# Kernel tuning notes

Measured on AMD Instinct MI355X. Metric: run time of the kernel, lower is better.

The kernel has to match this reference:

```python
import jax, jax.numpy as jnp
import numpy as np

EPS = 1e-12
SAMPLE_SIZES = (100, 50)  # hardcoded in the torch module


def setup_inputs() -> dict:
    key = jax.random.key(0)
    k1, k2, k3, k4 = jax.random.split(key, 4)
    N, E, C_IN, C_HID, C_OUT = 50000, 1600000, 256, 64, 128
    x = jax.random.normal(k1, (N, C_IN), dtype=jnp.float32)
    edge_index = jax.random.randint(k2, (2, E), 0, N, dtype=jnp.int64)
    W1 = jax.random.normal(k3, (C_IN, C_HID), dtype=jnp.float32) / np.sqrt(C_IN)
    b1 = jnp.zeros((C_HID,), dtype=jnp.float32)
    W2 = jax.random.normal(k4, (C_HID, C_OUT), dtype=jnp.float32) / np.sqrt(C_HID)
    b2 = jnp.zeros((C_OUT,), dtype=jnp.float32)
    return {"x": x, "edge_index": edge_index, "W1": W1, "b1": b1, "W2": W2, "b2": b2}


def _sample_mask(edge_index, num_samples, key):
    """Keep at most num_samples random out-edges per source node (fixed-shape mask)."""
    src = edge_index[0]
    E = src.shape[0]
    pri = jax.random.uniform(key, (E,))
    order = jnp.lexsort((pri, src))            # group by src, random order within group
    src_sorted = src[order]
    first = jnp.searchsorted(src_sorted, src_sorted, side="left")
    rank = jnp.arange(E) - first               # rank within each src group
    keep_sorted = rank < num_samples
    mask = jnp.zeros((E,), dtype=jnp.float32).at[order].set(keep_sorted.astype(jnp.float32))
    return mask


def _gcn_conv(x, edge_index, edge_weight, W, b, num_nodes):
    """PyG GCNConv: self-loops + symmetric deg^-1/2 normalization, aggregate at dst."""
    h = x @ W                                   # [N, out]
    src, dst = edge_index[0], edge_index[1]
    loop = jnp.arange(num_nodes, dtype=src.dtype)
    src_f = jnp.concatenate([src, loop])
    dst_f = jnp.concatenate([dst, loop])
    w_f = jnp.concatenate([edge_weight, jnp.ones((num_nodes,), dtype=edge_weight.dtype)])
    deg = jax.ops.segment_sum(w_f, dst_f, num_segments=num_nodes)
    dinv = jnp.where(deg > 0, jax.lax.rsqrt(jnp.maximum(deg, EPS)), 0.0)
    norm = w_f * dinv[src_f] * dinv[dst_f]      # [E+N]
    msgs = h[src_f] * norm[:, None]             # gather + scale (memory bound)
    out = jax.ops.segment_sum(msgs, dst_f, num_segments=num_nodes)
    return out + b


def reference(x, edge_index, W1, b1, W2, b2):
    num_nodes = x.shape[0]
    skey = jax.random.key(42)
    sk1, sk2 = jax.random.split(skey)
    m1 = _sample_mask(edge_index, SAMPLE_SIZES[0], sk1)
    m2 = _sample_mask(edge_index, SAMPLE_SIZES[1], sk2)
    h = _gcn_conv(x, edge_index, m1, W1, b1, num_nodes)
    h = jax.nn.relu(h)
    h = h / jnp.maximum(jnp.linalg.norm(h, axis=-1, keepdims=True), EPS)  # F.normalize(p=2)
    out = _gcn_conv(h, edge_index, m2, W2, b2, num_nodes)
    return out
```

## Files before the change

kernel.cpp:

```cpp
#include <hip/hip_runtime.h>

typedef unsigned int u32;
typedef unsigned short u16;
typedef unsigned long long u64;
typedef __attribute__((ext_vector_type(8))) short bh8;
typedef __attribute__((ext_vector_type(4))) float f4;

#define HMAX 1024
#define MAXD 128
#define SB_CAP 24576
#define SBCHUNK 2048
#define SPLIT 8

__device__ inline f4 mfma16(bh8 a, bh8 b, f4 c) {
  return __builtin_amdgcn_mfma_f32_16x16x32_bf16(a, b, c, 0, 0, 0);
}

__host__ __device__ inline void tf2x32(u32 k0, u32 k1, u32 x0, u32 x1, u32& o0, u32& o1) {
  u32 ks2 = k0 ^ k1 ^ 0x1BD11BDAu;
#define ROTL32(x,d) (((x)<<(d))|((x)>>(32-(d))))
#define TFR(r) { x0 += x1; x1 = ROTL32(x1,(r)); x1 ^= x0; }
  x0 += k0; x1 += k1;
  TFR(13) TFR(15) TFR(26) TFR(6)
  x0 += k1; x1 += ks2 + 1u;
  TFR(17) TFR(29) TFR(16) TFR(24)
  x0 += ks2; x1 += k0 + 2u;
  TFR(13) TFR(15) TFR(26) TFR(6)
  x0 += k0; x1 += k1 + 3u;
  TFR(17) TFR(29) TFR(16) TFR(24)
  x0 += k1; x1 += ks2 + 4u;
  TFR(13) TFR(15) TFR(26) TFR(6)
  x0 += ks2; x1 += k0 + 5u;
  o0 = x0; o1 = x1;
#undef TFR
#undef ROTL32
}

__device__ inline u16 f2bf(float f) {
  u32 u = __float_as_uint(f);
  return (u16)((u + 0x7FFFu + ((u >> 16) & 1u)) >> 16);
}
__device__ inline float bflo(u32 u) { return __uint_as_float(u << 16); }
__device__ inline float bfhi(u32 u) { return __uint_as_float(u & 0xFFFF0000u); }

__global__ __launch_bounds__(256) void k_prep(const float* __restrict__ W1, const float* __restrict__ W2,
                                              u16* __restrict__ W1t, u16* __restrict__ W2t) {
  int t = blockIdx.x * 256 + threadIdx.x;
  for (int e = t; e < 256 * 64; e += 1024) {
    int n = e & 63, k = e >> 6;
    W1t[n * 256 + k] = f2bf(W1[k * 64 + n]);
  }
  for (int e = t; e < 64 * 128; e += 1024) {
    int n = e & 127, k = e >> 7;
    W2t[n * 64 + k] = f2bf(W2[k * 128 + n]);
  }
}

__global__ __launch_bounds__(256) void k_srcbin(const int* __restrict__ ei,
                                                int* __restrict__ srcCnt, u32* __restrict__ srcRec,
                                                int* __restrict__ dstCnt, int E, int nb) {
  __shared__ u32 lsrc[128], ldst[128], lbase[128];
  int t = threadIdx.x;
  if (t < 128) { lsrc[t] = 0; ldst[t] = 0; }
  __syncthreads();
  int lo = blockIdx.x * SBCHUNK;
  int hi = min(lo + SBCHUNK, E);
  int sv[SBCHUNK / 256];
  int ci = 0;
  for (int i = lo + t; i < hi; i += 256) {
    int s = ei[i];
    int d = ei[E + i];
    sv[ci++] = s;
    atomicAdd(&lsrc[s >> 9], 1u);
    atomicAdd(&ldst[d >> 9], 1u);
  }
  __syncthreads();
  if (t < 128) {
    u32 c = lsrc[t];
    if (c) lbase[t] = (u32)atomicAdd(&srcCnt[t], (int)c);
    lsrc[t] = 0;
    if (ldst[t]) atomicAdd(&dstCnt[t], (int)ldst[t]);
  }
  __syncthreads();
  ci = 0;
  for (int i = lo + t; i < hi; i += 256) {
    int s = sv[ci++];
    int bk = s >> 9;
    u32 slot = lbase[bk] + atomicAdd(&lsrc[bk], 1u);
    if (slot < SB_CAP)
      srcRec[(size_t)bk * SB_CAP + slot] = ((u32)(s & 511) << 21) | (u32)i;
  }
}

__global__ __launch_bounds__(256) void k_shist(const int* __restrict__ srcCnt, const u32* __restrict__ srcRec,
                                               int* __restrict__ outdegB) {
  int bk = blockIdx.x >> 3;
  int part = blockIdx.x & (SPLIT - 1);
  int total = min(srcCnt[bk], SB_CAP);
  int lo = total * part / SPLIT;
  int hi = total * (part + 1) / SPLIT;
  __shared__ u32 cnt[512];
  int t = threadIdx.x;
  cnt[t] = 0; cnt[t + 256] = 0;
  __syncthreads();
  const u32* R = srcRec + (size_t)bk * SB_CAP;
  for (int i = lo + t; i < hi; i += 256) atomicAdd(&cnt[R[i] >> 21], 1u);
  __syncthreads();
  int base = bk * 512;
  for (int v = t; v < 512; v += 256) {
    u32 c = cnt[v];
    if (c) atomicAdd(&outdegB[base + v], (int)c);
  }
}

__global__ __launch_bounds__(256) void k_hdetect(const int* __restrict__ outdegB, u32* __restrict__ idAB,
                                                 int* __restrict__ hcA, int* __restrict__ hcB,
                                                 const int* __restrict__ dstCnt, int* __restrict__ bucketBase,
                                                 int* __restrict__ bucketCur, int* __restrict__ dptr,
                                                 int nb, int N) {
  if (blockIdx.x == 0 && threadIdx.x == 0) {
    int s = 0;
    for (int i = 0; i < nb; ++i) { bucketBase[i] = s; bucketCur[i] = s; s += dstCnt[i]; }
    bucketBase[nb] = s;
    dptr[N] = s;
  }
  int v = blockIdx.x * 256 + threadIdx.x;
  if (v >= N) return;
  int dg = outdegB[v];
  u32 pk = 0;
  if (dg > 50) {
    int idb = atomicAdd(hcB, 1);
    if (idb < HMAX) pk = (u32)(idb + 1);
    if (dg > 100) {
      int ida = atomicAdd(hcA, 1);
      if (ida < HMAX) pk |= (u32)(ida + 1) << 16;
    }
  }
  idAB[v] = pk;
}

__global__ __launch_bounds__(256) void k_hfill(const int* __restrict__ srcCnt, const u32* __restrict__ srcRec,
                                               const u32* __restrict__ idAB,
                                               int* __restrict__ bcA, u64* __restrict__ bukA,
                                               int* __restrict__ bcB, u64* __restrict__ bukB,
                                               u32 kaA, u32 kbA, u32 kaB, u32 kbB) {
  int bk = blockIdx.x >> 3;
  int part = blockIdx.x & (SPLIT - 1);
  int total = min(srcCnt[bk], SB_CAP);
  int lo = total * part / SPLIT;
  int hi = total * (part + 1) / SPLIT;
  const u32* R = srcRec + (size_t)bk * SB_CAP;
  int base = bk * 512;
  for (int i = lo + threadIdx.x; i < hi; i += 256) {
    u32 r = R[i];
    u32 pk = idAB[base + (int)(r >> 21)];
    if (pk) {
      u32 e = r & 0x1FFFFFu;
      int idb = (int)(pk & 0xFFFFu) - 1;
      if (idb >= 0) {
        u32 w0, w1; tf2x32(kaB, kbB, 0u, e, w0, w1);
        int slot = atomicAdd(&bcB[idb], 1);
        if (slot < MAXD) bukB[(size_t)idb * MAXD + slot] = ((u64)((w0 ^ w1) >> 9) << 32) | e;
      }
      int ida = (int)(pk >> 16) - 1;
      if (ida >= 0) {
        u32 w0, w1; tf2x32(kaA, kbA, 0u, e, w0, w1);
        int slot = atomicAdd(&bcA[ida], 1);
        if (slot < MAXD) bukA[(size_t)ida * MAXD + slot] = ((u64)((w0 ^ w1) >> 9) << 32) | e;
      }
    }
  }
}

__global__ __launch_bounds__(256) void k_rank2(const int* __restrict__ hcA, const int* __restrict__ bcA,
                                               const u64* __restrict__ bukA,
                                               const int* __restrict__ hcB, const int* __restrict__ bcB,
                                               const u64* __restrict__ bukB,
                                               unsigned char* __restrict__ mask) {
  bool isA = blockIdx.x < (HMAX / 4);
  int bx = isA ? blockIdx.x : blockIdx.x - HMAX / 4;
  const int* hcount = isA ? hcA : hcB;
  const int* bcount = isA ? bcA : bcB;
  const u64* bucket = isA ? bukA : bukB;
  int S = isA ? 100 : 50;
  int bit = isA ? 1 : 2;
  int wid = (bx * 256 + (int)threadIdx.x) >> 6;
  int lane = threadIdx.x & 63;
  int hc = hcount[0]; if (hc > HMAX) hc = HMAX;
  if (wid >= hc) return;
  int d = bcount[wid]; if (d > MAXD) d = MAXD;
  const u64* B = bucket + (size_t)wid * MAXD;
  for (int i = lane; i < d; i += 64) {
    u64 ki = B[i];
    int rank = 0;
    for (int j = 0; j < d; ++j) rank += (B[j] < ki) ? 1 : 0;
    if (rank >= S) {
      u32 e = (u32)ki;
      mask[e] = (unsigned char)(mask[e] & ~bit);
    }
  }
}

#define P1CHUNK 8192
__global__ __launch_bounds__(256) void k_phase1(const int* __restrict__ ei,
                                                const unsigned char* __restrict__ mask,
                                                int* __restrict__ bucketCur, u32* __restrict__ records, int E) {
  __shared__ u32 lc[128];
  __shared__ u32 lbase[128];
  int t = threadIdx.x;
  if (t < 128) lc[t] = 0;
  __syncthreads();
  int lo = blockIdx.x * P1CHUNK;
  int hi = min(lo + P1CHUNK, E);
  for (int i = lo + t; i < hi; i += 256) {
    int d = ei[E + i];
    atomicAdd(&lc[d >> 9], 1u);
  }
  __syncthreads();
  if (t < 128) {
    u32 c = lc[t];
    if (c) lbase[t] = (u32)atomicAdd(&bucketCur[t], (int)c);
    lc[t] = 0;
  }
  __syncthreads();
  for (int i = lo + t; i < hi; i += 256) {
    int s = ei[i];
    int d = ei[E + i];
    unsigned char m = mask[i];
    int bk = d >> 9;
    u32 slot = lbase[bk] + atomicAdd(&lc[bk], 1u);
    records[slot] = (u32)s | ((u32)(d & 511) << 16) | ((u32)(m & 3u) << 25);
  }
}

__global__ __launch_bounds__(256) void k_phase2(const int* __restrict__ bucketBase,
                                                const u32* __restrict__ records,
                                                u32* __restrict__ entries, int* __restrict__ dptr,
                                                float* __restrict__ dinv1, float* __restrict__ dinv2, int N) {
  int b = blockIdx.x;
  int lo = bucketBase[b], hi = bucketBase[b + 1];
  __shared__ u32 cnt[512];
  __shared__ u32 ws4[4];
  int t = threadIdx.x;
  cnt[t] = 0; cnt[t + 256] = 0;
  __syncthreads();
  for (int i = lo + t; i < hi; i += 256) {
    u32 r = records[i];
    u32 dl = (r >> 16) & 511u;
    u32 add = 1u + (((r >> 25) & 1u) << 10) + (((r >> 26) & 1u) << 20);
    atomicAdd(&cnt[dl], add);
  }
  __syncthreads();
  u32 c0 = cnt[2 * t], c1 = cnt[2 * t + 1];
  u32 n0 = c0 & 1023u, n1 = c1 & 1023u;
  u32 pair = n0 + n1;
  int lane = t & 63, w = t >> 6;
  u32 incl = pair;
  for (int off = 1; off < 64; off <<= 1) {
    u32 nbv = (u32)__shfl_up((int)incl, off, 64);
    if (lane >= off) incl += nbv;
  }
  if (lane == 63) ws4[w] = incl;
  __syncthreads();
  if (t == 0) { u32 s = 0; for (int k = 0; k < 4; ++k) { u32 x = ws4[k]; ws4[k] = s; s += x; } }
  __syncthreads();
  u32 excl = incl - pair + ws4[w];
  int v0 = b * 512 + 2 * t;
  if (v0 < N) {
    dptr[v0] = lo + (int)excl;
    dinv1[v0] = 1.0f / sqrtf((float)(((c0 >> 10) & 1023u) + 1u));
    dinv2[v0] = 1.0f / sqrtf((float)(((c0 >> 20) & 1023u) + 1u));
  }
  if (v0 + 1 < N) {
    dptr[v0 + 1] = lo + (int)(excl + n0);
    dinv1[v0 + 1] = 1.0f / sqrtf((float)(((c1 >> 10) & 1023u) + 1u));
    dinv2[v0 + 1] = 1.0f / sqrtf((float)(((c1 >> 20) & 1023u) + 1u));
  }
  __syncthreads();
  cnt[2 * t] = excl;
  cnt[2 * t + 1] = excl + n0;
  __syncthreads();
  for (int i = lo + t; i < hi; i += 256) {
    u32 r = records[i];
    u32 dl = (r >> 16) & 511u;
    u32 slot = atomicAdd(&cnt[dl], 1u);
    entries[lo + slot] = (r & 0xFFFFu) | ((r & (1u << 25)) ? (1u << 30) : 0u)
                                       | ((r & (1u << 26)) ? (1u << 31) : 0u);
  }
}

#define G1S 136
__global__ __launch_bounds__(256) void k_gemm1(const float* __restrict__ x, const u16* __restrict__ W1t,
                                               u16* __restrict__ h1b, int N) {
  __shared__ u16 xs[64 * G1S];
  __shared__ u16 ws[64 * G1S];
  int t = threadIdx.x;
  int wv = t >> 6, lane = t & 63;
  int qd = lane >> 4, md = lane & 15;
  int m0 = blockIdx.x * 64;
  f4 acc[4] = {};
  for (int ks = 0; ks < 256; ks += 128) {
    __syncthreads();
#pragma unroll
    for (int i = 0; i < 8; ++i) {
      int f = t + 256 * i;
      int r = f >> 5, c4 = f & 31;
      int grow = m0 + r; if (grow >= N) grow = N - 1;
      float4 v = ((const float4*)x)[(size_t)grow * 64 + (ks >> 2) + c4];
      u32 p0 = (u32)f2bf(v.x) | ((u32)f2bf(v.y) << 16);
      u32 p1 = (u32)f2bf(v.z) | ((u32)f2bf(v.w) << 16);
      *((uint2*)(xs + r * G1S + c4 * 4)) = make_uint2(p0, p1);
    }
#pragma unroll
    for (int i = 0; i < 4; ++i) {
      int cc = t + 256 * i;
      int n = cc >> 4, kc = (cc & 15) * 8;
      *((uint4*)(ws + n * G1S + kc)) = *((const uint4*)(W1t + n * 256 + ks + kc));
    }
    __syncthreads();
#pragma unroll
    for (int kk = 0; kk < 128; kk += 32) {
      bh8 af = *((const bh8*)(xs + (16 * wv + md) * G1S + kk + qd * 8));
#pragma unroll
      for (int nt = 0; nt < 4; ++nt) {
        bh8 bf = *((const bh8*)(ws + (nt * 16 + md) * G1S + kk + qd * 8));
        acc[nt] = mfma16(af, bf, acc[nt]);
      }
    }
  }
#pragma unroll
  for (int nt = 0; nt < 4; ++nt)
#pragma unroll
    for (int r = 0; r < 4; ++r) {
      int row = m0 + 16 * wv + qd * 4 + r;
      if (row < N) h1b[(size_t)row * 64 + nt * 16 + md] = f2bf(acc[nt][r]);
    }
}

__global__ __launch_bounds__(256) void k_conv1n(const int* __restrict__ ptr, const u32* __restrict__ entries,
                                                const float* __restrict__ dinv1, const uint4* __restrict__ h1q,
                                                const float* __restrict__ b1, uint4* __restrict__ hnbq, int N) {
  int wid = (blockIdx.x * 256 + threadIdx.x) >> 6;
  if (wid >= N) return;
  int lane = threadIdx.x & 63;
  int lo8 = lane & 7, grp = lane >> 3;
  int beg = ptr[wid], end = ptr[wid + 1];
  float a0 = 0.f, a1 = 0.f, a2 = 0.f, a3 = 0.f, a4 = 0.f, a5 = 0.f, a6 = 0.f, a7 = 0.f;
  for (int cb = beg; cb < end; cb += 64) {
    int idx = cb + lane;
    float wgt = 0.f; int s = 0;
    if (idx < end) {
      u32 e = entries[idx];
      s = (int)(e & 0xFFFFu);
      if (e & (1u << 30)) wgt = dinv1[s];
    }
    int nq = (min(64, end - cb) + 7) >> 3;
    int j = grp;
    float w = __shfl(wgt, j, 64);
    int sj = __shfl(s, j, 64);
    uint4 uv = h1q[(size_t)sj * 8 + lo8];
    for (int i = 1; i < nq; ++i) {
      int j2 = j + 8;
      float w2 = __shfl(wgt, j2, 64);
      int s2 = __shfl(s, j2, 64);
      uint4 uv2 = h1q[(size_t)s2 * 8 + lo8];
      a0 = fmaf(w, bflo(uv.x), a0); a1 = fmaf(w, bfhi(uv.x), a1);
      a2 = fmaf(w, bflo(uv.y), a2); a3 = fmaf(w, bfhi(uv.y), a3);
      a4 = fmaf(w, bflo(uv.z), a4); a5 = fmaf(w, bfhi(uv.z), a5);
      a6 = fmaf(w, bflo(uv.w), a6); a7 = fmaf(w, bfhi(uv.w), a7);
      w = w2; uv = uv2; j = j2;
    }
    a0 = fmaf(w, bflo(uv.x), a0); a1 = fmaf(w, bfhi(uv.x), a1);
    a2 = fmaf(w, bflo(uv.y), a2); a3 = fmaf(w, bfhi(uv.y), a3);
    a4 = fmaf(w, bflo(uv.z), a4); a5 = fmaf(w, bfhi(uv.z), a5);
    a6 = fmaf(w, bflo(uv.w), a6); a7 = fmaf(w, bfhi(uv.w), a7);
  }
#pragma unroll
  for (int off = 8; off < 64; off <<= 1) {
    a0 += __shfl_xor(a0, off, 64); a1 += __shfl_xor(a1, off, 64);
    a2 += __shfl_xor(a2, off, 64); a3 += __shfl_xor(a3, off, 64);
    a4 += __shfl_xor(a4, off, 64); a5 += __shfl_xor(a5, off, 64);
    a6 += __shfl_xor(a6, off, 64); a7 += __shfl_xor(a7, off, 64);
  }
  float dv = dinv1[wid];
  uint4 uo = h1q[(size_t)wid * 8 + lo8];
  a0 = fmaf(dv, bflo(uo.x), a0); a1 = fmaf(dv, bfhi(uo.x), a1);
  a2 = fmaf(dv, bflo(uo.y), a2); a3 = fmaf(dv, bfhi(uo.y), a3);
  a4 = fmaf(dv, bflo(uo.z), a4); a5 = fmaf(dv, bfhi(uo.z), a5);
  a6 = fmaf(dv, bflo(uo.w), a6); a7 = fmaf(dv, bfhi(uo.w), a7);
  float4 bbA = ((const float4*)b1)[lo8 * 2];
  float4 bbB = ((const float4*)b1)[lo8 * 2 + 1];
  float o0 = fmaxf(fmaf(dv, a0, bbA.x), 0.f);
  float o1 = fmaxf(fmaf(dv, a1, bbA.y), 0.f);
  float o2 = fmaxf(fmaf(dv, a2, bbA.z), 0.f);
  float o3 = fmaxf(fmaf(dv, a3, bbA.w), 0.f);
  float o4 = fmaxf(fmaf(dv, a4, bbB.x), 0.f);
  float o5 = fmaxf(fmaf(dv, a5, bbB.y), 0.f);
  float o6 = fmaxf(fmaf(dv, a6, bbB.z), 0.f);
  float o7 = fmaxf(fmaf(dv, a7, bbB.w), 0.f);
  float ss = fmaf(o0, o0, fmaf(o1, o1, fmaf(o2, o2, o3 * o3)))
           + fmaf(o4, o4, fmaf(o5, o5, fmaf(o6, o6, o7 * o7)));
#pragma unroll
  for (int off = 1; off < 8; off <<= 1) ss += __shfl_xor(ss, off, 8);
  float sc = 1.f / fmaxf(sqrtf(ss), 1e-12f);
  if (lane < 8) {
    uint4 pv;
    pv.x = (u32)f2bf(o0 * sc) | ((u32)f2bf(o1 * sc) << 16);
    pv.y = (u32)f2bf(o2 * sc) | ((u32)f2bf(o3 * sc) << 16);
    pv.z = (u32)f2bf(o4 * sc) | ((u32)f2bf(o5 * sc) << 16);
    pv.w = (u32)f2bf(o6 * sc) | ((u32)f2bf(o7 * sc) << 16);
    hnbq[(size_t)wid * 8 + lo8] = pv;
  }
}

__global__ __launch_bounds__(256) void k_agg2(const int* __restrict__ ptr, const u32* __restrict__ entries,
                                              const float* __restrict__ dinv2, const uint4* __restrict__ hnq,
                                              uint4* __restrict__ agg2q, int N) {
  int wid = (blockIdx.x * 256 + threadIdx.x) >> 6;
  if (wid >= N) return;
  int lane = threadIdx.x & 63;
  int lo8 = lane & 7, grp = lane >> 3;
  int beg = ptr[wid], end = ptr[wid + 1];
  float a0 = 0.f, a1 = 0.f, a2 = 0.f, a3 = 0.f, a4 = 0.f, a5 = 0.f, a6 = 0.f, a7 = 0.f;
  for (int cb = beg; cb < end; cb += 64) {
    int idx = cb + lane;
    float wgt = 0.f; int s = 0;
    if (idx < end) {
      u32 e = entries[idx];
      s = (int)(e & 0xFFFFu);
      if (e & (1u << 31)) wgt = dinv2[s];
    }
    int nq = (min(64, end - cb) + 7) >> 3;
    int j = grp;
    float w = __shfl(wgt, j, 64);
    int sj = __shfl(s, j, 64);
    uint4 uv = hnq[(size_t)sj * 8 + lo8];
    for (int i = 1; i < nq; ++i) {
      int j2 = j + 8;
      float w2 = __shfl(wgt, j2, 64);
      int s2 = __shfl(s, j2, 64);
      uint4 uv2 = hnq[(size_t)s2 * 8 + lo8];
      a0 = fmaf(w, bflo(uv.x), a0); a1 = fmaf(w, bfhi(uv.x), a1);
      a2 = fmaf(w, bflo(uv.y), a2); a3 = fmaf(w, bfhi(uv.y), a3);
      a4 = fmaf(w, bflo(uv.z), a4); a5 = fmaf(w, bfhi(uv.z), a5);
      a6 = fmaf(w, bflo(uv.w), a6); a7 = fmaf(w, bfhi(uv.w), a7);
      w = w2; uv = uv2; j = j2;
    }
    a0 = fmaf(w, bflo(uv.x), a0); a1 = fmaf(w, bfhi(uv.x), a1);
    a2 = fmaf(w, bflo(uv.y), a2); a3 = fmaf(w, bfhi(uv.y), a3);
    a4 = fmaf(w, bflo(uv.z), a4); a5 = fmaf(w, bfhi(uv.z), a5);
    a6 = fmaf(w, bflo(uv.w), a6); a7 = fmaf(w, bfhi(uv.w), a7);
  }
#pragma unroll
  for (int off = 8; off < 64; off <<= 1) {
    a0 += __shfl_xor(a0, off, 64); a1 += __shfl_xor(a1, off, 64);
    a2 += __shfl_xor(a2, off, 64); a3 += __shfl_xor(a3, off, 64);
    a4 += __shfl_xor(a4, off, 64); a5 += __shfl_xor(a5, off, 64);
    a6 += __shfl_xor(a6, off, 64); a7 += __shfl_xor(a7, off, 64);
  }
  float dv = dinv2[wid];
  uint4 uo = hnq[(size_t)wid * 8 + lo8];
  a0 = fmaf(dv, bflo(uo.x), a0); a1 = fmaf(dv, bfhi(uo.x), a1);
  a2 = fmaf(dv, bflo(uo.y), a2); a3 = fmaf(dv, bfhi(uo.y), a3);
  a4 = fmaf(dv, bflo(uo.z), a4); a5 = fmaf(dv, bfhi(uo.z), a5);
  a6 = fmaf(dv, bflo(uo.w), a6); a7 = fmaf(dv, bfhi(uo.w), a7);
  if (lane < 8) {
    uint4 pv;
    pv.x = (u32)f2bf(dv * a0) | ((u32)f2bf(dv * a1) << 16);
    pv.y = (u32)f2bf(dv * a2) | ((u32)f2bf(dv * a3) << 16);
    pv.z = (u32)f2bf(dv * a4) | ((u32)f2bf(dv * a5) << 16);
    pv.w = (u32)f2bf(dv * a6) | ((u32)f2bf(dv * a7) << 16);
    agg2q[(size_t)wid * 8 + lo8] = pv;
  }
}

#define G2S 72
__global__ __launch_bounds__(256) void k_gemm2f(const u16* __restrict__ aggb, const u16* __restrict__ W2t,
                                                const float* __restrict__ b2, float* __restrict__ out, int N) {
  __shared__ u16 hs[64 * G2S];
  __shared__ u16 ws[128 * G2S];
  int t = threadIdx.x;
  int wv = t >> 6, lane = t & 63;
  int qd = lane >> 4, md = lane & 15;
  int m0 = blockIdx.x * 64;
#pragma unroll
  for (int i = 0; i < 2; ++i) {
    int cc = t + 256 * i;
    int r = cc >> 3, kc = (cc & 7) * 8;
    int grow = m0 + r; if (grow >= N) grow = N - 1;
    *((uint4*)(hs + r * G2S + kc)) = *((const uint4*)(aggb + (size_t)grow * 64 + kc));
  }
#pragma unroll
  for (int i = 0; i < 4; ++i) {
    int cc = t + 256 * i;
    int n = cc >> 3, kc = (cc & 7) * 8;
    *((uint4*)(ws + n * G2S + kc)) = *((const uint4*)(W2t + n * 64 + kc));
  }
  __syncthreads();
  f4 acc[8] = {};
#pragma unroll
  for (int kk = 0; kk < 64; kk += 32) {
    bh8 af = *((const bh8*)(hs + (16 * wv + md) * G2S + kk + qd * 8));
#pragma unroll
    for (int nt = 0; nt < 8; ++nt) {
      bh8 bf = *((const bh8*)(ws + (nt * 16 + md) * G2S + kk + qd * 8));
      acc[nt] = mfma16(af, bf, acc[nt]);
    }
  }
#pragma unroll
  for (int nt = 0; nt < 8; ++nt) {
    float bv = b2[nt * 16 + md];
#pragma unroll
    for (int r = 0; r < 4; ++r) {
      int row = m0 + 16 * wv + qd * 4 + r;
      if (row < N) out[(size_t)row * 128 + nt * 16 + md] = acc[nt][r] + bv;
    }
  }
}

extern "C" void kernel_launch(void* const* d_in, const int* in_sizes, int n_in,
                              void* d_out, int out_size, void* d_ws, size_t ws_size,
                              hipStream_t stream) {
  const float* x  = (const float*)d_in[0];
  const int*   ei = (const int*)d_in[1];
  const float* W1 = (const float*)d_in[2];
  const float* b1 = (const float*)d_in[3];
  const float* W2 = (const float*)d_in[4];
  const float* b2 = (const float*)d_in[5];
  const int N = in_sizes[0] / 256;
  const int E = in_sizes[1] / 2;
  const int nb = (N + 511) >> 9;

  u32 sk1a, sk1b, sk2a, sk2b;
  tf2x32(0u, 42u, 0u, 0u, sk1a, sk1b);
  tf2x32(0u, 42u, 0u, 1u, sk2a, sk2b);

  char* p = (char*)d_ws;
  auto alloc = [&](size_t bytes) { char* r = p; p += (bytes + 255) & ~(size_t)255; return r; };
  int* dstCnt      = (int*)alloc(128 * 4);
  int* srcCnt      = (int*)alloc(128 * 4);
  int* hcbA        = (int*)alloc((size_t)(1 + HMAX) * 4);
  int* hcbB        = (int*)alloc((size_t)(1 + HMAX) * 4);
  int* outdegB     = (int*)alloc((size_t)nb * 512 * 4);
  char* zero_end = p;
  unsigned char* mask = (unsigned char*)alloc((size_t)E);
  u32* idAB     = (u32*)alloc((size_t)nb * 512 * 4);
  u16* h1b      = (u16*)alloc((size_t)N * 64 * 2);
  u16* hnb      = (u16*)alloc((size_t)N * 64 * 2);
  u16* agg2b    = (u16*)alloc((size_t)N * 64 * 2);
  float* dinv1  = (float*)alloc((size_t)N * 4);
  float* dinv2  = (float*)alloc((size_t)N * 4);
  int* dptr     = (int*)alloc((size_t)(N + 1) * 4);
  int* bucketBase = (int*)alloc(129 * 4);
  int* bucketCur  = (int*)alloc(128 * 4);
  u32* records  = (u32*)alloc((size_t)E * 4);
  u32* entries  = (u32*)alloc((size_t)E * 4);
  u32* srcRec   = (u32*)alloc((size_t)nb * SB_CAP * 4);
  u64* bukA     = (u64*)alloc((size_t)HMAX * MAXD * 8);
  u64* bukB     = (u64*)alloc((size_t)HMAX * MAXD * 8);
  u16* W1t      = (u16*)alloc(256 * 64 * 2);
  u16* W2t      = (u16*)alloc(64 * 128 * 2);

  int* hcA = hcbA; int* bcA = hcbA + 1;
  int* hcB = hcbB; int* bcB = hcbB + 1;

  hipMemsetAsync(dstCnt, 0x00, (size_t)(zero_end - (char*)dstCnt), stream);
  hipMemsetAsync(mask, 0x03, (size_t)E, stream);

  k_prep<<<4, 256, 0, stream>>>(W1, W2, W1t, W2t);
  k_srcbin<<<(E + SBCHUNK - 1) / SBCHUNK, 256, 0, stream>>>(ei, srcCnt, srcRec, dstCnt, E, nb);
  k_shist<<<nb * SPLIT, 256, 0, stream>>>(srcCnt, srcRec, outdegB);
  k_hdetect<<<(N + 255) / 256, 256, 0, stream>>>(outdegB, idAB, hcA, hcB, dstCnt, bucketBase,
                                                 bucketCur, dptr, nb, N);
  k_hfill<<<nb * SPLIT, 256, 0, stream>>>(srcCnt, srcRec, idAB, bcA, bukA, bcB, bukB,
                                          sk1a, sk1b, sk2a, sk2b);
  k_rank2<<<HMAX / 2, 256, 0, stream>>>(hcA, bcA, bukA, hcB, bcB, bukB, mask);
  k_phase1<<<(E + P1CHUNK - 1) / P1CHUNK, 256, 0, stream>>>(ei, mask, bucketCur, records, E);
  k_phase2<<<nb, 256, 0, stream>>>(bucketBase, records, entries, dptr, dinv1, dinv2, N);

  k_gemm1<<<(N + 63) / 64, 256, 0, stream>>>(x, W1t, h1b, N);
  k_conv1n<<<(N * 64 + 255) / 256, 256, 0, stream>>>(dptr, entries, dinv1, (const uint4*)h1b, b1,
                                                     (uint4*)hnb, N);
  k_agg2<<<(N * 64 + 255) / 256, 256, 0, stream>>>(dptr, entries, dinv2, (const uint4*)hnb,
                                                   (uint4*)agg2b, N);
  k_gemm2f<<<(N + 63) / 64, 256, 0, stream>>>(agg2b, W2t, b2, (float*)d_out, N);
}
```

Baseline: 313.3 us.

## Fuse edge binning, GEMM1 and weight prep into one heterogeneous kernel; drop phase1

Merges the src-binning kernel, the first GEMM and the W2 transpose into one launch, with blocks dispatched by index to different roles so the independent GEMM runs concurrently with the edge binning. The binning now also scatters destination-keyed records (dst, src, edge id) into capped per-bucket slots, which removes the separate phase1 pass that re-read the edge list. Phase2 reads the mask per edge via the stored edge id. W1 is transposed into shared memory inside the GEMM blocks, eliminating the prep kernel. The trade-offs are wider 64-bit records, a random mask gather, and truncation at SB_CAP per destination bucket.

```diff
diff --git a/kernel.cpp b/kernel.cpp
--- a/kernel.cpp
+++ b/kernel.cpp
@@ -11,6 +11,7 @@
 #define SB_CAP 24576
 #define SBCHUNK 2048
 #define SPLIT 8
+#define G1S 136
 
 __device__ inline f4 mfma16(bh8 a, bh8 b, f4 c) {
   return __builtin_amdgcn_mfma_f32_16x16x32_bf16(a, b, c, 0, 0, 0);
@@ -43,52 +44,116 @@
 __device__ inline float bflo(u32 u) { return __uint_as_float(u << 16); }
 __device__ inline float bfhi(u32 u) { return __uint_as_float(u & 0xFFFF0000u); }
 
-__global__ __launch_bounds__(256) void k_prep(const float* __restrict__ W1, const float* __restrict__ W2,
-                                              u16* __restrict__ W1t, u16* __restrict__ W2t) {
-  int t = blockIdx.x * 256 + threadIdx.x;
-  for (int e = t; e < 256 * 64; e += 1024) {
-    int n = e & 63, k = e >> 6;
-    W1t[n * 256 + k] = f2bf(W1[k * 64 + n]);
-  }
-  for (int e = t; e < 64 * 128; e += 1024) {
-    int n = e & 127, k = e >> 7;
-    W2t[n * 64 + k] = f2bf(W2[k * 128 + n]);
-  }
-}
-
-__global__ __launch_bounds__(256) void k_srcbin(const int* __restrict__ ei,
-                                                int* __restrict__ srcCnt, u32* __restrict__ srcRec,
-                                                int* __restrict__ dstCnt, int E, int nb) {
-  __shared__ u32 lsrc[128], ldst[128], lbase[128];
+struct BinS { u32 lsrc[128]; u32 lbase[128]; u32 ldst[128]; u32 dbase[128]; };
+struct GemS { u16 xs[64 * G1S]; u16 ws[64 * G1S]; };
+
+__global__ __launch_bounds__(256) void k_mega1(const int* __restrict__ ei, int E,
+                                               const float* __restrict__ x, int N,
+                                               const float* __restrict__ W1, const float* __restrict__ W2,
+                                               int* __restrict__ srcCnt, u32* __restrict__ srcRec,
+                                               int* __restrict__ dstCnt, u64* __restrict__ dstRec,
+                                               u16* __restrict__ h1b, u16* __restrict__ W2t, int nBin) {
+  __shared__ __align__(16) char smem[sizeof(GemS)];
   int t = threadIdx.x;
-  if (t < 128) { lsrc[t] = 0; ldst[t] = 0; }
-  __syncthreads();
-  int lo = blockIdx.x * SBCHUNK;
-  int hi = min(lo + SBCHUNK, E);
-  int sv[SBCHUNK / 256];
-  int ci = 0;
-  for (int i = lo + t; i < hi; i += 256) {
-    int s = ei[i];
-    int d = ei[E + i];
-    sv[ci++] = s;
-    atomicAdd(&lsrc[s >> 9], 1u);
-    atomicAdd(&ldst[d >> 9], 1u);
-  }
-  __syncthreads();
-  if (t < 128) {
-    u32 c = lsrc[t];
-    if (c) lbase[t] = (u32)atomicAdd(&srcCnt[t], (int)c);
-    lsrc[t] = 0;
-    if (ldst[t]) atomicAdd(&dstCnt[t], (int)ldst[t]);
-  }
-  __syncthreads();
-  ci = 0;
-  for (int i = lo + t; i < hi; i += 256) {
-    int s = sv[ci++];
-    int bk = s >> 9;
-    u32 slot = lbase[bk] + atomicAdd(&lsrc[bk], 1u);
-    if (slot < SB_CAP)
-      srcRec[(size_t)bk * SB_CAP + slot] = ((u32)(s & 511) << 21) | (u32)i;
+  int bid = blockIdx.x;
+
+  if (bid < nBin) {
+    BinS& S = *(BinS*)smem;
+    if (t < 128) { S.lsrc[t] = 0; S.ldst[t] = 0; }
+    __syncthreads();
+    int lo = bid * SBCHUNK;
+    int hi = min(lo + SBCHUNK, E);
+    int e0 = lo + 8 * t;
+    int nv = min(8, hi - e0); if (nv < 0) nv = 0;
+    int sv[8], dv[8];
+    if (nv == 8 && ((E & 3) == 0)) {
+      int4 a0 = *((const int4*)(ei + e0));
+      int4 a1 = *((const int4*)(ei + e0 + 4));
+      int4 b0 = *((const int4*)(ei + E + e0));
+      int4 b1 = *((const int4*)(ei + E + e0 + 4));
+      sv[0]=a0.x; sv[1]=a0.y; sv[2]=a0.z; sv[3]=a0.w; sv[4]=a1.x; sv[5]=a1.y; sv[6]=a1.z; sv[7]=a1.w;
+      dv[0]=b0.x; dv[1]=b0.y; dv[2]=b0.z; dv[3]=b0.w; dv[4]=b1.x; dv[5]=b1.y; dv[6]=b1.z; dv[7]=b1.w;
+    } else {
+      for (int j = 0; j < nv; ++j) { sv[j] = ei[e0 + j]; dv[j] = ei[E + e0 + j]; }
+    }
+    for (int j = 0; j < nv; ++j) {
+      atomicAdd(&S.lsrc[sv[j] >> 9], 1u);
+      atomicAdd(&S.ldst[dv[j] >> 9], 1u);
+    }
+    __syncthreads();
+    if (t < 128) {
+      u32 c = S.lsrc[t];
+      if (c) S.lbase[t] = (u32)atomicAdd(&srcCnt[t], (int)c);
+      S.lsrc[t] = 0;
+      u32 cd = S.ldst[t];
+      if (cd) S.dbase[t] = (u32)atomicAdd(&dstCnt[t], (int)cd);
+      S.ldst[t] = 0;
+    }
+    __syncthreads();
+    for (int j = 0; j < nv; ++j) {
+      int s = sv[j], d = dv[j];
+      u32 i = (u32)(e0 + j);
+      int bs = s >> 9;
+      u32 slot = S.lbase[bs] + atomicAdd(&S.lsrc[bs], 1u);
+      if (slot < SB_CAP) srcRec[(size_t)bs * SB_CAP + slot] = ((u32)(s & 511) << 21) | i;
+      int bd = d >> 9;
+      u32 slot2 = S.dbase[bd] + atomicAdd(&S.ldst[bd], 1u);
+      if (slot2 < SB_CAP)
+        dstRec[(size_t)bd * SB_CAP + slot2] = ((u64)(d & 511) << 37) | ((u64)(u32)s << 21) | i;
+    }
+  } else if (bid < 2 * nBin) {
+    GemS& G = *(GemS*)smem;
+    int wv = t >> 6, lane = t & 63;
+    int qd = lane >> 4, md = lane & 15;
+    int m0 = (bid - nBin) * 64;
+    if (m0 >= N) return;
+    f4 acc[4] = {};
+    for (int ks = 0; ks < 256; ks += 128) {
+      __syncthreads();
+#pragma unroll
+      for (int i = 0; i < 8; ++i) {
+        int f = t + 256 * i;
+        int r = f >> 5, c4 = f & 31;
+        int grow = m0 + r; if (grow >= N) grow = N - 1;
+        float4 v = ((const float4*)x)[(size_t)grow * 64 + (ks >> 2) + c4];
+        u32 p0 = (u32)f2bf(v.x) | ((u32)f2bf(v.y) << 16);
+        u32 p1 = (u32)f2bf(v.z) | ((u32)f2bf(v.w) << 16);
+        *((uint2*)(G.xs + r * G1S + c4 * 4)) = make_uint2(p0, p1);
+      }
+#pragma unroll
+      for (int i = 0; i < 8; ++i) {
+        int f = t + 256 * i;
+        int k = f >> 4, c4 = f & 15;
+        float4 v = ((const float4*)W1)[(ks + k) * 16 + c4];
+        int n0 = c4 * 4;
+        G.ws[(n0 + 0) * G1S + k] = f2bf(v.x);
+        G.ws[(n0 + 1) * G1S + k] = f2bf(v.y);
+        G.ws[(n0 + 2) * G1S + k] = f2bf(v.z);
+        G.ws[(n0 + 3) * G1S + k] = f2bf(v.w);
+      }
+      __syncthreads();
+#pragma unroll
+      for (int kk = 0; kk < 128; kk += 32) {
+        bh8 af = *((const bh8*)(G.xs + (16 * wv + md) * G1S + kk + qd * 8));
+#pragma unroll
+        for (int nt = 0; nt < 4; ++nt) {
+          bh8 bf = *((const bh8*)(G.ws + (nt * 16 + md) * G1S + kk + qd * 8));
+          acc[nt] = mfma16(af, bf, acc[nt]);
+        }
+      }
+    }
+#pragma unroll
+    for (int nt = 0; nt < 4; ++nt)
+#pragma unroll
+      for (int r = 0; r < 4; ++r) {
+        int row = m0 + 16 * wv + qd * 4 + r;
+        if (row < N) h1b[(size_t)row * 64 + nt * 16 + md] = f2bf(acc[nt][r]);
+      }
+  } else {
+    for (int e = t; e < 64 * 128; e += 256) {
+      int n = e & 127, k = e >> 7;
+      W2t[n * 64 + k] = f2bf(W2[k * 128 + n]);
+    }
   }
 }
 
@@ -116,11 +181,10 @@
 __global__ __launch_bounds__(256) void k_hdetect(const int* __restrict__ outdegB, u32* __restrict__ idAB,
                                                  int* __restrict__ hcA, int* __restrict__ hcB,
                                                  const int* __restrict__ dstCnt, int* __restrict__ bucketBase,
-                                                 int* __restrict__ bucketCur, int* __restrict__ dptr,
-                                                 int nb, int N) {
+                                                 int* __restrict__ dptr, int nb, int N) {
   if (blockIdx.x == 0 && threadIdx.x == 0) {
     int s = 0;
-    for (int i = 0; i < nb; ++i) { bucketBase[i] = s; bucketCur[i] = s; s += dstCnt[i]; }
+    for (int i = 0; i < nb; ++i) { bucketBase[i] = s; s += min(dstCnt[i], SB_CAP); }
     bucketBase[nb] = s;
     dptr[N] = s;
   }
@@ -201,53 +265,26 @@
   }
 }
 
-#define P1CHUNK 8192
-__global__ __launch_bounds__(256) void k_phase1(const int* __restrict__ ei,
+__global__ __launch_bounds__(256) void k_phase2(const int* __restrict__ bucketBase,
+                                                const int* __restrict__ dstCnt,
+                                                const u64* __restrict__ dstRec,
                                                 const unsigned char* __restrict__ mask,
-                                                int* __restrict__ bucketCur, u32* __restrict__ records, int E) {
-  __shared__ u32 lc[128];
-  __shared__ u32 lbase[128];
-  int t = threadIdx.x;
-  if (t < 128) lc[t] = 0;
-  __syncthreads();
-  int lo = blockIdx.x * P1CHUNK;
-  int hi = min(lo + P1CHUNK, E);
-  for (int i = lo + t; i < hi; i += 256) {
-    int d = ei[E + i];
-    atomicAdd(&lc[d >> 9], 1u);
-  }
-  __syncthreads();
-  if (t < 128) {
-    u32 c = lc[t];
-    if (c) lbase[t] = (u32)atomicAdd(&bucketCur[t], (int)c);
-    lc[t] = 0;
-  }
-  __syncthreads();
-  for (int i = lo + t; i < hi; i += 256) {
-    int s = ei[i];
-    int d = ei[E + i];
-    unsigned char m = mask[i];
-    int bk = d >> 9;
-    u32 slot = lbase[bk] + atomicAdd(&lc[bk], 1u);
-    records[slot] = (u32)s | ((u32)(d & 511) << 16) | ((u32)(m & 3u) << 25);
-  }
-}
-
-__global__ __launch_bounds__(256) void k_phase2(const int* __restrict__ bucketBase,
-                                                const u32* __restrict__ records,
                                                 u32* __restrict__ entries, int* __restrict__ dptr,
                                                 float* __restrict__ dinv1, float* __restrict__ dinv2, int N) {
   int b = blockIdx.x;
-  int lo = bucketBase[b], hi = bucketBase[b + 1];
+  int base = bucketBase[b];
+  int cnt0 = min(dstCnt[b], SB_CAP);
+  const u64* R = dstRec + (size_t)b * SB_CAP;
   __shared__ u32 cnt[512];
   __shared__ u32 ws4[4];
   int t = threadIdx.x;
   cnt[t] = 0; cnt[t + 256] = 0;
   __syncthreads();
-  for (int i = lo + t; i < hi; i += 256) {
-    u32 r = records[i];
-    u32 dl = (r >> 16) & 511u;
-    u32 add = 1u + (((r >> 25) & 1u) << 10) + (((r >> 26) & 1u) << 20);
+  for (int i = t; i < cnt0; i += 256) {
+    u64 r = R[i];
+    u32 dl = (u32)(r >> 37) & 511u;
+    u32 m = mask[(u32)r & 0x1FFFFFu];
+    u32 add = 1u + ((m & 1u) << 10) + (((m >> 1) & 1u) << 20);
     atomicAdd(&cnt[dl], add);
   }
   __syncthreads();
@@ -267,12 +304,12 @@
   u32 excl = incl - pair + ws4[w];
   int v0 = b * 512 + 2 * t;
   if (v0 < N) {
-    dptr[v0] = lo + (int)excl;
+    dptr[v0] = base + (int)excl;
     dinv1[v0] = 1.0f / sqrtf((float)(((c0 >> 10) & 1023u) + 1u));
     dinv2[v0] = 1.0f / sqrtf((float)(((c0 >> 20) & 1023u) + 1u));
   }
   if (v0 + 1 < N) {
-    dptr[v0 + 1] = lo + (int)(excl + n0);
+    dptr[v0 + 1] = base + (int)(excl + n0);
     dinv1[v0 + 1] = 1.0f / sqrtf((float)(((c1 >> 10) & 1023u) + 1u));
     dinv2[v0 + 1] = 1.0f / sqrtf((float)(((c1 >> 20) & 1023u) + 1u));
   }
@@ -280,61 +317,14 @@
   cnt[2 * t] = excl;
   cnt[2 * t + 1] = excl + n0;
   __syncthreads();
-  for (int i = lo + t; i < hi; i += 256) {
-    u32 r = records[i];
-    u32 dl = (r >> 16) & 511u;
+  for (int i = t; i < cnt0; i += 256) {
+    u64 r = R[i];
+    u32 dl = (u32)(r >> 37) & 511u;
+    u32 m = mask[(u32)r & 0x1FFFFFu];
+    u32 src = (u32)(r >> 21) & 0xFFFFu;
     u32 slot = atomicAdd(&cnt[dl], 1u);
-    entries[lo + slot] = (r & 0xFFFFu) | ((r & (1u << 25)) ? (1u << 30) : 0u)
-                                       | ((r & (1u << 26)) ? (1u << 31) : 0u);
-  }
-}
-
-#define G1S 136
-__global__ __launch_bounds__(256) void k_gemm1(const float* __restrict__ x, const u16* __restrict__ W1t,
-                                               u16* __restrict__ h1b, int N) {
-  __shared__ u16 xs[64 * G1S];
-  __shared__ u16 ws[64 * G1S];
-  int t = threadIdx.x;
-  int wv = t >> 6, lane = t & 63;
-  int qd = lane >> 4, md = lane & 15;
-  int m0 = blockIdx.x * 64;
-  f4 acc[4] = {};
-  for (int ks = 0; ks < 256; ks += 128) {
-    __syncthreads();
-#pragma unroll
-    for (int i = 0; i < 8; ++i) {
-      int f = t + 256 * i;
-      int r = f >> 5, c4 = f & 31;
-      int grow = m0 + r; if (grow >= N) grow = N - 1;
-      float4 v = ((const float4*)x)[(size_t)grow * 64 + (ks >> 2) + c4];
-      u32 p0 = (u32)f2bf(v.x) | ((u32)f2bf(v.y) << 16);
-      u32 p1 = (u32)f2bf(v.z) | ((u32)f2bf(v.w) << 16);
-      *((uint2*)(xs + r * G1S + c4 * 4)) = make_uint2(p0, p1);
-    }
-#pragma unroll
-    for (int i = 0; i < 4; ++i) {
-      int cc = t + 256 * i;
-      int n = cc >> 4, kc = (cc & 15) * 8;
-      *((uint4*)(ws + n * G1S + kc)) = *((const uint4*)(W1t + n * 256 + ks + kc));
-    }
-    __syncthreads();
-#pragma unroll
-    for (int kk = 0; kk < 128; kk += 32) {
-      bh8 af = *((const bh8*)(xs + (16 * wv + md) * G1S + kk + qd * 8));
-#pragma unroll
-      for (int nt = 0; nt < 4; ++nt) {
-        bh8 bf = *((const bh8*)(ws + (nt * 16 + md) * G1S + kk + qd * 8));
-        acc[nt] = mfma16(af, bf, acc[nt]);
-      }
-    }
-  }
-#pragma unroll
-  for (int nt = 0; nt < 4; ++nt)
-#pragma unroll
-    for (int r = 0; r < 4; ++r) {
-      int row = m0 + 16 * wv + qd * 4 + r;
-      if (row < N) h1b[(size_t)row * 64 + nt * 16 + md] = f2bf(acc[nt][r]);
-    }
+    entries[base + slot] = src | ((m & 1u) ? (1u << 30) : 0u) | ((m & 2u) ? (1u << 31) : 0u);
+  }
 }
 
 __global__ __launch_bounds__(256) void k_conv1n(const int* __restrict__ ptr, const u32* __restrict__ entries,
@@ -552,13 +542,11 @@
   float* dinv2  = (float*)alloc((size_t)N * 4);
   int* dptr     = (int*)alloc((size_t)(N + 1) * 4);
   int* bucketBase = (int*)alloc(129 * 4);
-  int* bucketCur  = (int*)alloc(128 * 4);
-  u32* records  = (u32*)alloc((size_t)E * 4);
   u32* entries  = (u32*)alloc((size_t)E * 4);
   u32* srcRec   = (u32*)alloc((size_t)nb * SB_CAP * 4);
+  u64* dstRec   = (u64*)alloc((size_t)nb * SB_CAP * 8);
   u64* bukA     = (u64*)alloc((size_t)HMAX * MAXD * 8);
   u64* bukB     = (u64*)alloc((size_t)HMAX * MAXD * 8);
-  u16* W1t      = (u16*)alloc(256 * 64 * 2);
   u16* W2t      = (u16*)alloc(64 * 128 * 2);
 
   int* hcA = hcbA; int* bcA = hcbA + 1;
@@ -567,18 +555,18 @@
   hipMemsetAsync(dstCnt, 0x00, (size_t)(zero_end - (char*)dstCnt), stream);
   hipMemsetAsync(mask, 0x03, (size_t)E, stream);
 
-  k_prep<<<4, 256, 0, stream>>>(W1, W2, W1t, W2t);
-  k_srcbin<<<(E + SBCHUNK - 1) / SBCHUNK, 256, 0, stream>>>(ei, srcCnt, srcRec, dstCnt, E, nb);
+  const int nBin = (E + SBCHUNK - 1) / SBCHUNK;
+  const int nGemm = (N + 63) / 64;
+  k_mega1<<<nBin + nGemm + 1, 256, 0, stream>>>(ei, E, x, N, W1, W2,
+                                                srcCnt, srcRec, dstCnt, dstRec, h1b, W2t, nBin);
   k_shist<<<nb * SPLIT, 256, 0, stream>>>(srcCnt, srcRec, outdegB);
   k_hdetect<<<(N + 255) / 256, 256, 0, stream>>>(outdegB, idAB, hcA, hcB, dstCnt, bucketBase,
-                                                 bucketCur, dptr, nb, N);
+                                                 dptr, nb, N);
   k_hfill<<<nb * SPLIT, 256, 0, stream>>>(srcCnt, srcRec, idAB, bcA, bukA, bcB, bukB,
                                           sk1a, sk1b, sk2a, sk2b);
   k_rank2<<<HMAX / 2, 256, 0, stream>>>(hcA, bcA, bukA, hcB, bcB, bukB, mask);
-  k_phase1<<<(E + P1CHUNK - 1) / P1CHUNK, 256, 0, stream>>>(ei, mask, bucketCur, records, E);
-  k_phase2<<<nb, 256, 0, stream>>>(bucketBase, records, entries, dptr, dinv1, dinv2, N);
-
-  k_gemm1<<<(N + 63) / 64, 256, 0, stream>>>(x, W1t, h1b, N);
+  k_phase2<<<nb, 256, 0, stream>>>(bucketBase, dstCnt, dstRec, mask, entries, dptr,
+                                   dinv1, dinv2, N);
   k_conv1n<<<(N * 64 + 255) / 256, 256, 0, stream>>>(dptr, entries, dinv1, (const uint4*)h1b, b1,
                                                      (uint4*)hnb, N);
   k_agg2<<<(N * 64 + 255) / 256, 256, 0, stream>>>(dptr, entries, dinv2, (const uint4*)hnb,
```

New measurement: 333.4 us. +6.4%, slower.
